# Kernel tuning notes

Hardware: AMD Instinct MI355X
Metric: run time of the kernel (lower is better)

## Reference

```python
import jax, jax.numpy as jnp
import numpy as np
from jax import lax

QK_K = 256          # elements per Q6_K super-block
TYPE_SIZE = 210     # bytes per Q6_K super-block (128 ql + 64 qh + 16 scales + 2 d)
OUT_F = 14336
IN_F = 4096


def setup_inputs() -> dict:
    key = jax.random.key(0)
    kx, kb = jax.random.split(key)
    x = jax.random.normal(kx, (16, 1, IN_F), dtype=jnp.float32)
    bias = jax.random.normal(kb, (OUT_F,), dtype=jnp.float32) * 0.02

    # Build realistic packed Q6_K weight bytes with numpy (bit packing).
    rng = np.random.default_rng(0)
    n_blocks = OUT_F * IN_F // QK_K
    ql = rng.integers(0, 256, (n_blocks, 128), dtype=np.uint8)
    qh = rng.integers(0, 256, (n_blocks, 64), dtype=np.uint8)
    scales = rng.integers(-32, 32, (n_blocks, 16)).astype(np.int8).view(np.uint8)
    d = (rng.standard_normal(n_blocks) * 0.004).astype(np.float16).view(np.uint8).reshape(n_blocks, 2)
    w_q = jnp.asarray(np.concatenate([ql, qh, scales, d], axis=1))  # [n_blocks, 210] uint8
    return {"x": x, "w_q": w_q, "bias": bias}


def _dequant_q6_k(w_q, out_f, in_f):
    # w_q: [n_blocks, 210] uint8 -> [out_f, in_f] float32
    n = w_q.shape[0]
    ql = w_q[:, :128].astype(jnp.int32)
    qh = w_q[:, 128:192].astype(jnp.int32)
    sc = lax.bitcast_convert_type(w_q[:, 192:208], jnp.int8).astype(jnp.float32)  # [n,16]
    d_u16 = w_q[:, 208].astype(jnp.uint16) | (w_q[:, 209].astype(jnp.uint16) << 8)
    d = lax.bitcast_convert_type(d_u16, jnp.float16).astype(jnp.float32)          # [n]
    dl = (d[:, None] * sc).reshape(n, 16, 1)                                      # per-16-elt scale

    shift_l = jnp.array([0, 4], dtype=jnp.int32).reshape(1, 1, 2, 1)
    ql = ((ql.reshape(n, 2, 1, 64) >> shift_l) & 15).reshape(n, 8, 32)
    shift_h = jnp.array([0, 2, 4, 6], dtype=jnp.int32).reshape(1, 1, 4, 1)
    qh = ((qh.reshape(n, 2, 1, 32) >> shift_h) & 3).reshape(n, 8, 32)
    q = (ql | (qh << 4)) - 32                                                     # int in [-32, 31]
    w = dl * q.reshape(n, 16, 16).astype(jnp.float32)
    return w.reshape(out_f, in_f)


def reference(x, w_q, bias):
    in_f = x.shape[-1]
    out_f = bias.shape[0]
    w = _dequant_q6_k(w_q, out_f, in_f)          # [out_f, in_f]
    return jnp.einsum("bsi,oi->bso", x, w) + bias
```

## Files before the change

kernel.cpp:

```cpp
#include <hip/hip_runtime.h>
#include <hip/hip_bf16.h>
#include <hip/hip_fp16.h>
#include <stdint.h>


#define OUT_F 14336
#define IN_F  4096
#define NB    16

using f32x4  = __attribute__((ext_vector_type(4))) float;
using short8 = __attribute__((ext_vector_type(8))) short;

typedef const __attribute__((address_space(1))) void* gas1_t;
typedef __attribute__((address_space(3))) void* las3_t;

__device__ __forceinline__ void gload16(const uint32_t* g, uint32_t* l) {
  __builtin_amdgcn_global_load_lds((gas1_t)g, (las3_t)l, 16, 0, 0);
}
__device__ __forceinline__ void gload4(const uint32_t* g, uint32_t* l) {
  __builtin_amdgcn_global_load_lds((gas1_t)g, (las3_t)l, 4, 0, 0);
}

__device__ __forceinline__ uint32_t pack_bf16(float lo, float hi) {
  return (__builtin_bit_cast(uint32_t, lo) >> 16) |
         (__builtin_bit_cast(uint32_t, hi) & 0xffff0000u);
}

__global__ __launch_bounds__(256)
void prep_kernel(const float* __restrict__ x, const float* __restrict__ bias,
                 float* __restrict__ out, ushort* __restrict__ xbf, int use_ws)
{
  const int t = blockIdx.x * 256 + threadIdx.x;
  if (t < NB * OUT_F) {
    out[t] = bias[t % OUT_F];
  }
  if (use_ws && t < NB * IN_F) {
    uint32_t u = __builtin_bit_cast(uint32_t, x[t]);
    xbf[t] = (ushort)((u + 0x8000u) >> 16);
  }
}

constexpr int ROW_DW = 212;
constexpr int ROW_B  = ROW_DW * 4;
constexpr int BUF_B  = 16 * ROW_B;

template<bool USE_WS>
__global__ __launch_bounds__(256, 5)
void q6k_gemm(const uint32_t* __restrict__ wq,
              const float* __restrict__ xf,
              const ushort* __restrict__ xbf,
              float* __restrict__ out)
{
  __shared__ __align__(16) uint8_t wlds[2][BUF_B];

  const int tid  = threadIdx.x;
  const int lane = tid & 63;
  const int wv   = tid >> 6;
  const int l15  = lane & 15;
  const int lg   = lane >> 4;
  const int bx   = blockIdx.x;
  const int by   = blockIdx.y;
  const int row_base = bx * 16;
  const int sb0 = by * 8;

  f32x4 acc = {0.f, 0.f, 0.f, 0.f};

  auto stage = [&](int buf, int ph) {
    const size_t gb = (size_t)row_base * 3360 + (size_t)(sb0 + ph) * 210;
    #pragma unroll
    for (int i = 0; i < 4; ++i) {
      const int r = wv * 4 + i;
      const uint32_t* g = wq + gb + (size_t)r * 3360;
      uint32_t* l = (uint32_t*)(&wlds[buf][r * ROW_B]);
      if (lane < 52) gload16(g + lane * 4, l);
      if (lane < 2)  gload4(g + 208 + lane, l + 208);
    }
  };

  auto compute = [&](int buf, int ph) {
    const uint8_t* rb = &wlds[buf][l15 * ROW_B];
    const uint2 dd = *(const uint2*)(rb + 832);
    const float dsup = __half2float(__builtin_bit_cast(__half,
                       (uint16_t)((dd.x & 0xffu) | ((dd.y & 0xffu) << 8))));
    #pragma unroll
    for (int mm = 0; mm < 2; ++mm) {
      const int m = 2 * wv + mm;
      const uint8_t* qlp = rb + (m >> 2) * 256 + (m & 1) * 128 + lg * 32;
      const uint8_t* qhp = rb + 512 + (m >> 2) * 128 + lg * 32;
      const uint4 A0 = *(const uint4*)(qlp);
      const uint4 A1 = *(const uint4*)(qlp + 16);
      const uint4 B0 = *(const uint4*)(qhp);
      const uint4 B1 = *(const uint4*)(qhp + 16);
      const uint32_t scd = *(const uint32_t*)(rb + 768 + 8 * m + 4 * (lg >> 1));

      const float dl  = dsup * (float)(int)(int8_t)(uint8_t)scd;
      const float mdl = -32.0f * dl;
      const int SL = 4 * ((m >> 1) & 1);
      const int SH = 2 * (m & 3);
      auto dq = [&](uint32_t q, uint32_t h) -> float {
        const uint32_t t = ((q >> SL) & 15u) | (((h >> SH) & 3u) << 4);
        return fmaf((float)t, dl, mdl);
      };

      union { short8 s; uint32_t u[4]; } bfr;
      bfr.u[0] = pack_bf16(dq(A0.x, B0.x), dq(A0.y, B0.y));
      bfr.u[1] = pack_bf16(dq(A0.z, B0.z), dq(A0.w, B0.w));
      bfr.u[2] = pack_bf16(dq(A1.x, B1.x), dq(A1.y, B1.y));
      bfr.u[3] = pack_bf16(dq(A1.z, B1.z), dq(A1.w, B1.w));

      const int k0 = by * 2048 + ph * 256 + m * 32 + lg * 8;
      short8 afrag;
      if constexpr (USE_WS) {
        afrag = *(const short8*)(xbf + (size_t)l15 * IN_F + k0);
      } else {
        const float* xp = xf + (size_t)l15 * IN_F + k0;
        const f32x4 v0 = *(const f32x4*)(xp);
        const f32x4 v1 = *(const f32x4*)(xp + 4);
        union { short8 s; uint32_t u[4]; } av;
        av.u[0] = pack_bf16(v0[0], v0[1]);
        av.u[1] = pack_bf16(v0[2], v0[3]);
        av.u[2] = pack_bf16(v1[0], v1[1]);
        av.u[3] = pack_bf16(v1[2], v1[3]);
        afrag = av.s;
      }

      acc = __builtin_amdgcn_mfma_f32_16x16x32_bf16(afrag, bfr.s, acc, 0, 0, 0);
    }
  };

  stage(0, 0);
  __syncthreads();
  #pragma unroll
  for (int p = 0; p < 8; ++p) {
    if (p < 7) stage((p + 1) & 1, p + 1);
    compute(p & 1, p);
    __syncthreads();
  }

  float (*red)[64][4] = (float (*)[64][4])(&wlds[0][0]);
  *(f32x4*)(&red[wv][lane][0]) = acc;
  __syncthreads();

  const int b  = tid >> 4;
  const int r0 = tid & 15;
  const int ls = (b >> 2) * 16 + r0;
  const int rg = b & 3;
  const float sum = red[0][ls][rg] + red[1][ls][rg] + red[2][ls][rg] + red[3][ls][rg];
  atomicAdd(&out[(size_t)b * OUT_F + row_base + r0], sum);
}

extern "C" void kernel_launch(void* const* d_in, const int* in_sizes, int n_in,
                              void* d_out, int out_size, void* d_ws, size_t ws_size,
                              hipStream_t stream)
{
  const float*    x    = (const float*)d_in[0];
  const uint32_t* wq   = (const uint32_t*)d_in[1];
  const float*    bias = (const float*)d_in[2];
  float*  out = (float*)d_out;
  ushort* xbf = (ushort*)d_ws;
  const bool use_ws = ws_size >= (size_t)NB * IN_F * 2;

  prep_kernel<<<dim3(896), dim3(256), 0, stream>>>(x, bias, out, xbf, use_ws ? 1 : 0);

  dim3 grid(OUT_F / 16, 2);
  if (use_ws) {
    q6k_gemm<true><<<grid, dim3(256), 0, stream>>>(wq, x, xbf, out);
  } else {
    q6k_gemm<false><<<grid, dim3(256), 0, stream>>>(wq, x, xbf, out);
  }
}
```

Measured before the change: 43.41 us.

## Drop prep kernel: memset output, fold bias into GEMM, convert x inline

Removes the separate prep kernel that wrote bias into the output and converted x to bf16 in workspace. The output is now zeroed with an async memset, the by==0 blocks add the bias before their atomic add, and x is always read as fp32 and packed to bf16 inside the GEMM. The per-superblock fp16 scale is now read straight from global memory instead of being staged into LDS with an extra 4-byte async load. This trades one kernel launch and a pass over the output for more redundant global reads of x and d, plus a memset node.

Measured after the change: 56.78 us. 30.8% more time.

```diff
diff --git a/kernel.cpp b/kernel.cpp
--- a/kernel.cpp
+++ b/kernel.cpp
@@ -17,38 +17,20 @@
 __device__ __forceinline__ void gload16(const uint32_t* g, uint32_t* l) {
   __builtin_amdgcn_global_load_lds((gas1_t)g, (las3_t)l, 16, 0, 0);
 }
-__device__ __forceinline__ void gload4(const uint32_t* g, uint32_t* l) {
-  __builtin_amdgcn_global_load_lds((gas1_t)g, (las3_t)l, 4, 0, 0);
-}
 
 __device__ __forceinline__ uint32_t pack_bf16(float lo, float hi) {
   return (__builtin_bit_cast(uint32_t, lo) >> 16) |
          (__builtin_bit_cast(uint32_t, hi) & 0xffff0000u);
 }
 
-__global__ __launch_bounds__(256)
-void prep_kernel(const float* __restrict__ x, const float* __restrict__ bias,
-                 float* __restrict__ out, ushort* __restrict__ xbf, int use_ws)
-{
-  const int t = blockIdx.x * 256 + threadIdx.x;
-  if (t < NB * OUT_F) {
-    out[t] = bias[t % OUT_F];
-  }
-  if (use_ws && t < NB * IN_F) {
-    uint32_t u = __builtin_bit_cast(uint32_t, x[t]);
-    xbf[t] = (ushort)((u + 0x8000u) >> 16);
-  }
-}
-
 constexpr int ROW_DW = 212;
 constexpr int ROW_B  = ROW_DW * 4;
 constexpr int BUF_B  = 16 * ROW_B;
 
-template<bool USE_WS>
 __global__ __launch_bounds__(256, 5)
 void q6k_gemm(const uint32_t* __restrict__ wq,
               const float* __restrict__ xf,
-              const ushort* __restrict__ xbf,
+              const float* __restrict__ bias,
               float* __restrict__ out)
 {
   __shared__ __align__(16) uint8_t wlds[2][BUF_B];
@@ -73,13 +55,13 @@
       const uint32_t* g = wq + gb + (size_t)r * 3360;
       uint32_t* l = (uint32_t*)(&wlds[buf][r * ROW_B]);
       if (lane < 52) gload16(g + lane * 4, l);
-      if (lane < 2)  gload4(g + 208 + lane, l + 208);
     }
   };
 
   auto compute = [&](int buf, int ph) {
     const uint8_t* rb = &wlds[buf][l15 * ROW_B];
-    const uint2 dd = *(const uint2*)(rb + 832);
+    const uint2 dd = *(const uint2*)(wq + (size_t)(row_base + l15) * 3360 +
+                                     (size_t)(sb0 + ph) * 210 + 208);
     const float dsup = __half2float(__builtin_bit_cast(__half,
                        (uint16_t)((dd.x & 0xffu) | ((dd.y & 0xffu) << 8))));
     #pragma unroll
@@ -109,22 +91,16 @@
       bfr.u[3] = pack_bf16(dq(A1.z, B1.z), dq(A1.w, B1.w));
 
       const int k0 = by * 2048 + ph * 256 + m * 32 + lg * 8;
-      short8 afrag;
-      if constexpr (USE_WS) {
-        afrag = *(const short8*)(xbf + (size_t)l15 * IN_F + k0);
-      } else {
-        const float* xp = xf + (size_t)l15 * IN_F + k0;
-        const f32x4 v0 = *(const f32x4*)(xp);
-        const f32x4 v1 = *(const f32x4*)(xp + 4);
-        union { short8 s; uint32_t u[4]; } av;
-        av.u[0] = pack_bf16(v0[0], v0[1]);
-        av.u[1] = pack_bf16(v0[2], v0[3]);
-        av.u[2] = pack_bf16(v1[0], v1[1]);
-        av.u[3] = pack_bf16(v1[2], v1[3]);
-        afrag = av.s;
-      }
+      const float* xp = xf + (size_t)l15 * IN_F + k0;
+      const f32x4 v0 = *(const f32x4*)(xp);
+      const f32x4 v1 = *(const f32x4*)(xp + 4);
+      union { short8 s; uint32_t u[4]; } av;
+      av.u[0] = pack_bf16(v0[0], v0[1]);
+      av.u[1] = pack_bf16(v0[2], v0[3]);
+      av.u[2] = pack_bf16(v1[0], v1[1]);
+      av.u[3] = pack_bf16(v1[2], v1[3]);
 
-      acc = __builtin_amdgcn_mfma_f32_16x16x32_bf16(afrag, bfr.s, acc, 0, 0, 0);
+      acc = __builtin_amdgcn_mfma_f32_16x16x32_bf16(av.s, bfr.s, acc, 0, 0, 0);
     }
   };
 
@@ -145,8 +121,10 @@
   const int r0 = tid & 15;
   const int ls = (b >> 2) * 16 + r0;
   const int rg = b & 3;
-  const float sum = red[0][ls][rg] + red[1][ls][rg] + red[2][ls][rg] + red[3][ls][rg];
-  atomicAdd(&out[(size_t)b * OUT_F + row_base + r0], sum);
+  float sum = red[0][ls][rg] + red[1][ls][rg] + red[2][ls][rg] + red[3][ls][rg];
+  const int orow = row_base + r0;
+  if (by == 0) sum += bias[orow];
+  atomicAdd(&out[(size_t)b * OUT_F + orow], sum);
 }
 
 extern "C" void kernel_launch(void* const* d_in, const int* in_sizes, int n_in,
@@ -156,16 +134,10 @@
   const float*    x    = (const float*)d_in[0];
   const uint32_t* wq   = (const uint32_t*)d_in[1];
   const float*    bias = (const float*)d_in[2];
-  float*  out = (float*)d_out;
-  ushort* xbf = (ushort*)d_ws;
-  const bool use_ws = ws_size >= (size_t)NB * IN_F * 2;
+  float* out = (float*)d_out;
 
-  prep_kernel<<<dim3(896), dim3(256), 0, stream>>>(x, bias, out, xbf, use_ws ? 1 : 0);
+  hipMemsetAsync(out, 0, (size_t)out_size * sizeof(float), stream);
 
   dim3 grid(OUT_F / 16, 2);
-  if (use_ws) {
-    q6k_gemm<true><<<grid, dim3(256), 0, stream>>>(wq, x, xbf, out);
-  } else {
-    q6k_gemm<false><<<grid, dim3(256), 0, stream>>>(wq, x, xbf, out);
-  }
+  q6k_gemm<<<grid, dim3(256), 0, stream>>>(wq, x, bias, out);
 }
```

## Drop split-K, fuse bias into epilogue and remove atomic accumulation

Applied to the files above, without the earlier changes.

Each block now covers the full K dimension (16 phases) instead of splitting K across two blocks. This lets the epilogue write output plus bias directly, with no atomicAdd and no bias pre-initialisation of the output in the prep kernel. The grid is halved to 896 blocks, which lowers parallelism and lengthens the serial pipeline per block. In exchange it removes the atomics and the extra output write pass.

Result: no change. 43.92 us (+1.2%).

```diff
diff --git a/kernel.cpp b/kernel.cpp
--- a/kernel.cpp
+++ b/kernel.cpp
@@ -27,14 +27,10 @@
 }
 
 __global__ __launch_bounds__(256)
-void prep_kernel(const float* __restrict__ x, const float* __restrict__ bias,
-                 float* __restrict__ out, ushort* __restrict__ xbf, int use_ws)
+void prep_kernel(const float* __restrict__ x, ushort* __restrict__ xbf)
 {
   const int t = blockIdx.x * 256 + threadIdx.x;
-  if (t < NB * OUT_F) {
-    out[t] = bias[t % OUT_F];
-  }
-  if (use_ws && t < NB * IN_F) {
+  if (t < NB * IN_F) {
     uint32_t u = __builtin_bit_cast(uint32_t, x[t]);
     xbf[t] = (ushort)((u + 0x8000u) >> 16);
   }
@@ -43,12 +39,14 @@
 constexpr int ROW_DW = 212;
 constexpr int ROW_B  = ROW_DW * 4;
 constexpr int BUF_B  = 16 * ROW_B;
+constexpr int NP     = 16;
 
 template<bool USE_WS>
 __global__ __launch_bounds__(256, 5)
 void q6k_gemm(const uint32_t* __restrict__ wq,
               const float* __restrict__ xf,
               const ushort* __restrict__ xbf,
+              const float* __restrict__ bias,
               float* __restrict__ out)
 {
   __shared__ __align__(16) uint8_t wlds[2][BUF_B];
@@ -58,15 +56,12 @@
   const int wv   = tid >> 6;
   const int l15  = lane & 15;
   const int lg   = lane >> 4;
-  const int bx   = blockIdx.x;
-  const int by   = blockIdx.y;
-  const int row_base = bx * 16;
-  const int sb0 = by * 8;
+  const int row_base = blockIdx.x * 16;
 
   f32x4 acc = {0.f, 0.f, 0.f, 0.f};
 
   auto stage = [&](int buf, int ph) {
-    const size_t gb = (size_t)row_base * 3360 + (size_t)(sb0 + ph) * 210;
+    const size_t gb = (size_t)row_base * 3360 + (size_t)ph * 210;
     #pragma unroll
     for (int i = 0; i < 4; ++i) {
       const int r = wv * 4 + i;
@@ -108,7 +103,7 @@
       bfr.u[2] = pack_bf16(dq(A1.x, B1.x), dq(A1.y, B1.y));
       bfr.u[3] = pack_bf16(dq(A1.z, B1.z), dq(A1.w, B1.w));
 
-      const int k0 = by * 2048 + ph * 256 + m * 32 + lg * 8;
+      const int k0 = ph * 256 + m * 32 + lg * 8;
       short8 afrag;
       if constexpr (USE_WS) {
         afrag = *(const short8*)(xbf + (size_t)l15 * IN_F + k0);
@@ -131,8 +126,8 @@
   stage(0, 0);
   __syncthreads();
   #pragma unroll
-  for (int p = 0; p < 8; ++p) {
-    if (p < 7) stage((p + 1) & 1, p + 1);
+  for (int p = 0; p < NP; ++p) {
+    if (p < NP - 1) stage((p + 1) & 1, p + 1);
     compute(p & 1, p);
     __syncthreads();
   }
@@ -146,7 +141,8 @@
   const int ls = (b >> 2) * 16 + r0;
   const int rg = b & 3;
   const float sum = red[0][ls][rg] + red[1][ls][rg] + red[2][ls][rg] + red[3][ls][rg];
-  atomicAdd(&out[(size_t)b * OUT_F + row_base + r0], sum);
+  const int orow = row_base + r0;
+  out[(size_t)b * OUT_F + orow] = sum + bias[orow];
 }
 
 extern "C" void kernel_launch(void* const* d_in, const int* in_sizes, int n_in,
@@ -160,12 +156,10 @@
   ushort* xbf = (ushort*)d_ws;
   const bool use_ws = ws_size >= (size_t)NB * IN_F * 2;
 
-  prep_kernel<<<dim3(896), dim3(256), 0, stream>>>(x, bias, out, xbf, use_ws ? 1 : 0);
-
-  dim3 grid(OUT_F / 16, 2);
   if (use_ws) {
-    q6k_gemm<true><<<grid, dim3(256), 0, stream>>>(wq, x, xbf, out);
+    prep_kernel<<<dim3((NB * IN_F + 255) / 256), dim3(256), 0, stream>>>(x, xbf);
+    q6k_gemm<true><<<dim3(OUT_F / 16), dim3(256), 0, stream>>>(wq, x, xbf, bias, out);
   } else {
-    q6k_gemm<false><<<grid, dim3(256), 0, stream>>>(wq, x, xbf, out);
+    q6k_gemm<false><<<dim3(OUT_F / 16), dim3(256), 0, stream>>>(wq, x, xbf, bias, out);
   }
 }
```
